# Performance work log

Measured on AMD Instinct MI355X. Metric: run time of the kernel, lower is better.

Reference implementation:

```python
import jax, jax.numpy as jnp
import numpy as np

NEG = -9e15
ALPHA = 0.2  # leaky relu slope

def setup_inputs() -> dict:
    key = jax.random.key(0)
    k1, k2, k3, k4 = jax.random.split(key, 4)
    N, Fin, Fout = 8192, 512, 256
    h = jax.random.normal(k1, (N, Fin), dtype=jnp.float32)
    adj = jax.random.randint(k2, (N, N), 0, 2, dtype=jnp.int32)
    # xavier_uniform with gain=1.414
    gain = 1.414
    limW = gain * np.sqrt(6.0 / (Fin + Fout))
    W = jax.random.uniform(k3, (Fin, Fout), dtype=jnp.float32, minval=-limW, maxval=limW)
    lima = gain * np.sqrt(6.0 / (2 * Fout + 1))
    a = jax.random.uniform(k4, (2 * Fout, 1), dtype=jnp.float32, minval=-lima, maxval=lima)
    return {"h": h, "adj": adj, "W": W, "a": a}

def reference(h, adj, W, a):
    Fout = W.shape[1]
    Wh = h @ W                                   # [N, Fout]
    # decompose a = [a1; a2]: e_ij = leaky(a1.Wh_i + a2.Wh_j)
    f1 = Wh @ a[:Fout]                           # [N, 1]
    f2 = Wh @ a[Fout:]                           # [N, 1]
    e = jax.nn.leaky_relu(f1 + f2.T, negative_slope=ALPHA)  # [N, N]
    e = jnp.where(adj > 0, e, jnp.float32(NEG))
    attention = jax.nn.softmax(e, axis=1)
    # dropout is identity at inference (training=False)
    h_prime = attention @ Wh                     # [N, Fout]
    return jax.nn.elu(h_prime)
```

## Files before the change

### kernel.cpp

```cpp
#include <hip/hip_runtime.h>
#include <cstdint>
#include <cstddef>

#define ALPHA 0.2f

typedef __attribute__((ext_vector_type(8)))  short short8;
typedef __attribute__((ext_vector_type(16))) float f32x16;

static __device__ __forceinline__ unsigned short f2bf(float x) {
  union { float f; unsigned u; } c; c.f = x;
  unsigned u = c.u;
  unsigned r = (u + 0x7FFFu + ((u >> 16) & 1u)) >> 16;
  return (unsigned short)r;
}
static __device__ __forceinline__ float bf2f(unsigned short b) {
  union { unsigned u; float f; } c; c.u = ((unsigned)b) << 16;
  return c.f;
}

__global__ __launch_bounds__(256, 2) void gemm1(const float* __restrict__ h,
                                                const float* __restrict__ W,
                                                float* __restrict__ Wh) {
  __shared__ float As[32][132];
  __shared__ float Bs[32][64];
  const int t = threadIdx.x;
  const int bid = blockIdx.x;
  const int nb = bid & 3, mb = bid >> 2;
  const int m0 = mb * 128, n0 = nb * 64;
  const int ty = t >> 4, tx = t & 15;
  float acc[8][4];
#pragma unroll
  for (int i = 0; i < 8; i++)
#pragma unroll
    for (int j = 0; j < 4; j++) acc[i][j] = 0.f;

  for (int k0 = 0; k0 < 512; k0 += 32) {
#pragma unroll
    for (int c = 0; c < 4; c++) {
      int m = c * 32 + (t >> 3);
      int kq = (t & 7) * 4;
      float4 v = *(const float4*)&h[(size_t)(m0 + m) * 512 + k0 + kq];
      As[kq + 0][m] = v.x; As[kq + 1][m] = v.y;
      As[kq + 2][m] = v.z; As[kq + 3][m] = v.w;
    }
#pragma unroll
    for (int c = 0; c < 2; c++) {
      int k = c * 16 + (t >> 4);
      int n = (t & 15) * 4;
      *(float4*)&Bs[k][n] = *(const float4*)&W[(size_t)(k0 + k) * 256 + n0 + n];
    }
    __syncthreads();
#pragma unroll
    for (int k = 0; k < 32; k++) {
      float4 a0 = *(float4*)&As[k][ty * 8];
      float4 a1 = *(float4*)&As[k][ty * 8 + 4];
      float4 b  = *(float4*)&Bs[k][tx * 4];
      float av[8] = {a0.x, a0.y, a0.z, a0.w, a1.x, a1.y, a1.z, a1.w};
      float bv[4] = {b.x, b.y, b.z, b.w};
#pragma unroll
      for (int i = 0; i < 8; i++)
#pragma unroll
        for (int j = 0; j < 4; j++) acc[i][j] = fmaf(av[i], bv[j], acc[i][j]);
    }
    __syncthreads();
  }
#pragma unroll
  for (int i = 0; i < 8; i++) {
    float4 v = {acc[i][0], acc[i][1], acc[i][2], acc[i][3]};
    *(float4*)&Wh[(size_t)(m0 + ty * 8 + i) * 256 + n0 + tx * 4] = v;
  }
}

__global__ __launch_bounds__(256) void rowstats(const float* __restrict__ Wh,
                                                const float* __restrict__ a,
                                                float* __restrict__ f1,
                                                float* __restrict__ f2,
                                                unsigned* __restrict__ uvpack) {
  const int t = threadIdx.x;
  const int w = t >> 6, lane = t & 63;
  const int i = blockIdx.x * 4 + w;
  float4 wv = *(const float4*)&Wh[(size_t)i * 256 + lane * 4];
  float4 a1 = *(const float4*)&a[lane * 4];
  float4 a2 = *(const float4*)&a[256 + lane * 4];
  float s1 = wv.x * a1.x + wv.y * a1.y + wv.z * a1.z + wv.w * a1.w;
  float s2 = wv.x * a2.x + wv.y * a2.y + wv.z * a2.z + wv.w * a2.w;
#pragma unroll
  for (int off = 32; off; off >>= 1) { s1 += __shfl_xor(s1, off); s2 += __shfl_xor(s2, off); }
  if (lane == 0) {
    f1[i] = s1; f2[i] = s2;
    float u = __expf(s2), v = __expf(ALPHA * s2);
    uvpack[i] = (unsigned)f2bf(u) | ((unsigned)f2bf(v) << 16);
  }
}

__global__ __launch_bounds__(256) void wtrans(const float* __restrict__ Wh,
                                              unsigned short* __restrict__ WhT) {
  __shared__ unsigned short T[64][80];
  const int t = threadIdx.x;
  const int bi = blockIdx.x & 127;
  const int bc = blockIdx.x >> 7;
  const int i0 = bi * 64, c0 = bc * 64;
  {
    const int il = t >> 2, cq = (t & 3) * 16;
#pragma unroll
    for (int k = 0; k < 4; ++k) {
      float4 v = *(const float4*)&Wh[(size_t)(i0 + il) * 256 + c0 + cq + k * 4];
      T[cq + k * 4 + 0][il] = f2bf(v.x);
      T[cq + k * 4 + 1][il] = f2bf(v.y);
      T[cq + k * 4 + 2][il] = f2bf(v.z);
      T[cq + k * 4 + 3][il] = f2bf(v.w);
    }
  }
  __syncthreads();
  {
    const int cl = t >> 2, iq = (t & 3) * 16;
    *(uint4*)&WhT[(size_t)(c0 + cl) * 8192 + i0 + iq]     = *(const uint4*)&T[cl][iq];
    *(uint4*)&WhT[(size_t)(c0 + cl) * 8192 + i0 + iq + 8] = *(const uint4*)&T[cl][iq + 8];
  }
}

__global__ __launch_bounds__(256) void f2max_k(const float* __restrict__ f2,
                                               float* __restrict__ f2maxp) {
  __shared__ float red[256];
  const int t = threadIdx.x;
  float m = -1e30f;
  for (int c = 0; c < 32; c++) m = fmaxf(m, f2[c * 256 + t]);
  red[t] = m;
  __syncthreads();
  for (int s = 128; s; s >>= 1) {
    if (t < s) red[t] = fmaxf(red[t], red[t + s]);
    __syncthreads();
  }
  if (t == 0) f2maxp[0] = red[0];
}

#define ATTN_PHASE(S_CUR, A0, A1, U0, U1, BF_CUR, BF_NXT)                        \
  {                                                                              \
    const int ad_[8] = {A0.x, A0.y, A0.z, A0.w, A1.x, A1.y, A1.z, A1.w};         \
    const unsigned uu_[8] = {U0.x, U0.y, U0.z, U0.w, U1.x, U1.y, U1.z, U1.w};    \
    float w_[8];                                                                 \
    _Pragma("unroll")                                                            \
    for (int jj = 0; jj < 8; jj++) {                                             \
      float u = bf2f((unsigned short)(uu_[jj] & 0xFFFFu));                       \
      float v = bf2f((unsigned short)(uu_[jj] >> 16));                           \
      float wv = (u > Ui) ? Ai * u : Bi * v;                                     \
      w_[jj] = (ad_[jj] > 0) ? wv : 0.f;                                         \
    }                                                                            \
    lpriv += ((w_[0] + w_[1]) + (w_[2] + w_[3])) + ((w_[4] + w_[5]) + (w_[6] + w_[7])); \
    union { uint4 q; short8 s; } af_;                                            \
    asm("v_cvt_pk_bf16_f32 %0, %1, %2" : "=v"(af_.q.x) : "v"(w_[0]), "v"(w_[1]));\
    asm("v_cvt_pk_bf16_f32 %0, %1, %2" : "=v"(af_.q.y) : "v"(w_[2]), "v"(w_[3]));\
    asm("v_cvt_pk_bf16_f32 %0, %1, %2" : "=v"(af_.q.z) : "v"(w_[4]), "v"(w_[5]));\
    asm("v_cvt_pk_bf16_f32 %0, %1, %2" : "=v"(af_.q.w) : "v"(w_[6]), "v"(w_[7]));\
    const int sRe_ = (S_CUR) + 2;                                                \
    if (sRe_ < 128) {                                                            \
      A0 = *(const int4*)(adjp + sRe_ * 16);                                     \
      A1 = *(const int4*)(adjp + sRe_ * 16 + 4);                                 \
      U0 = *(const uint4*)(uvp + sRe_ * 16);                                     \
      U1 = *(const uint4*)(uvp + sRe_ * 16 + 4);                                 \
    }                                                                            \
    const int sN_ = (S_CUR) + 1;                                                 \
    if (sN_ < 128) {                                                             \
      _Pragma("unroll")                                                          \
      for (int ct = 0; ct < 8; ct++)                                             \
        BF_NXT[ct] = *(const short8*)(wtp + (size_t)ct * (32 * 8192) + sN_ * 16);\
    }                                                                            \
    _Pragma("unroll")                                                            \
    for (int ct = 0; ct < 8; ct++)                                               \
      acc[ct] = __builtin_amdgcn_mfma_f32_32x32x16_bf16(af_.s, BF_CUR[ct], acc[ct], 0, 0, 0); \
  }

__global__ __launch_bounds__(256, 1) void attn_main(const int* __restrict__ adj,
                                                    const float* __restrict__ f1,
                                                    const unsigned* __restrict__ uvpack,
                                                    const unsigned short* __restrict__ WhT,
                                                    const float* __restrict__ f2maxp,
                                                    float* __restrict__ out) {
  __shared__ float red[4][32][260];
  __shared__ float lsum[4][32];
  const int t = threadIdx.x;
  const int wave = t >> 6, lane = t & 63;
  const int am = lane & 31, asel = lane >> 5;
  const int r0 = blockIdx.x * 32;
  const int row = r0 + am;
  const int jq = wave * 2048;
  const int joff = jq + asel * 8;

  const float F2max = f2maxp[0];
  const float f1v = f1[row];
  const float x = f1v + F2max;
  const float M = x > 0.f ? x : ALPHA * x;
  const float Ai = __expf(f1v - M);
  const float Bi = __expf(ALPHA * f1v - M);
  const float Ui = __expf(-f1v);

  f32x16 acc[8] = {};
  const int* adjp = adj + (size_t)row * 8192 + joff;
  const unsigned* uvp = uvpack + joff;
  const unsigned short* wtp = WhT + (size_t)am * 8192 + joff;

  int4 aA0 = *(const int4*)(adjp);
  int4 aA1 = *(const int4*)(adjp + 4);
  uint4 uA0 = *(const uint4*)(uvp);
  uint4 uA1 = *(const uint4*)(uvp + 4);
  int4 aB0 = *(const int4*)(adjp + 16);
  int4 aB1 = *(const int4*)(adjp + 20);
  uint4 uB0 = *(const uint4*)(uvp + 16);
  uint4 uB1 = *(const uint4*)(uvp + 20);
  short8 bfA[8], bfB[8];
#pragma unroll
  for (int ct = 0; ct < 8; ct++)
    bfA[ct] = *(const short8*)(wtp + (size_t)ct * (32 * 8192));
  float lpriv = 0.f;

#pragma unroll 1
  for (int it = 0; it < 64; ++it) {
    ATTN_PHASE(2 * it,     aA0, aA1, uA0, uA1, bfA, bfB);
    ATTN_PHASE(2 * it + 1, aB0, aB1, uB0, uB1, bfB, bfA);
  }

#pragma unroll
  for (int ct = 0; ct < 8; ct++) {
#pragma unroll
    for (int reg = 0; reg < 16; reg++) {
      const int rowl = (reg & 3) + 8 * (reg >> 2) + 4 * asel;
      red[wave][rowl][ct * 32 + am] = acc[ct][reg];
    }
  }
  lpriv += __shfl_xor(lpriv, 32);
  if (asel == 0) lsum[wave][am] = lpriv;
  __syncthreads();

  const int rr = t >> 3, cb = (t & 7) * 32;
  const float l = lsum[0][rr] + lsum[1][rr] + lsum[2][rr] + lsum[3][rr];
  const float inv = 1.0f / fmaxf(l, 1e-30f);
#pragma unroll
  for (int cc = 0; cc < 32; cc += 4) {
    float4 v;
    v.x = red[0][rr][cb + cc + 0] + red[1][rr][cb + cc + 0] + red[2][rr][cb + cc + 0] + red[3][rr][cb + cc + 0];
    v.y = red[0][rr][cb + cc + 1] + red[1][rr][cb + cc + 1] + red[2][rr][cb + cc + 1] + red[3][rr][cb + cc + 1];
    v.z = red[0][rr][cb + cc + 2] + red[1][rr][cb + cc + 2] + red[2][rr][cb + cc + 2] + red[3][rr][cb + cc + 2];
    v.w = red[0][rr][cb + cc + 3] + red[1][rr][cb + cc + 3] + red[2][rr][cb + cc + 3] + red[3][rr][cb + cc + 3];
    v.x *= inv; v.y *= inv; v.z *= inv; v.w *= inv;
    float4 o;
    o.x = v.x > 0.f ? v.x : __expf(v.x) - 1.f;
    o.y = v.y > 0.f ? v.y : __expf(v.y) - 1.f;
    o.z = v.z > 0.f ? v.z : __expf(v.z) - 1.f;
    o.w = v.w > 0.f ? v.w : __expf(v.w) - 1.f;
    *(float4*)&out[(size_t)(r0 + rr) * 256 + cb + cc] = o;
  }
}

extern "C" void kernel_launch(void* const* d_in, const int* in_sizes, int n_in,
                              void* d_out, int out_size, void* d_ws, size_t ws_size,
                              hipStream_t stream) {
  const float* h  = (const float*)d_in[0];
  const int* adj  = (const int*)d_in[1];
  const float* W  = (const float*)d_in[2];
  const float* a  = (const float*)d_in[3];
  float* out = (float*)d_out;
  char* ws = (char*)d_ws;

  float* Wh            = (float*)ws;
  unsigned short* WhT  = (unsigned short*)(ws + (size_t)(16u << 20));
  float* f1            = (float*)(ws + (size_t)(20u << 20));
  float* f2            = (float*)(ws + (size_t)(20u << 20) + (32u << 10));
  unsigned* uvpack     = (unsigned*)(ws + (size_t)(20u << 20) + (64u << 10));
  float* f2maxp        = (float*)(ws + (size_t)(20u << 20) + (96u << 10));

  gemm1<<<256, 256, 0, stream>>>(h, W, Wh);
  rowstats<<<2048, 256, 0, stream>>>(Wh, a, f1, f2, uvpack);
  wtrans<<<512, 256, 0, stream>>>(Wh, WhT);
  f2max_k<<<1, 256, 0, stream>>>(f2, f2maxp);
  attn_main<<<256, 256, 0, stream>>>(adj, f1, uvpack, WhT, f2maxp, out);
}
```

Before: 570.4 us.

## Pre-pack adjacency into bitmask, restructure attention loop, and widen gemm1 blocks

A new maskpack kernel reads the int32 adjacency once with coalesced loads and ballots it into a 64-bit-per-64-column bitmask. attn_main then streams this compact mask instead of 32-bit adj values, and applies it with bit-extract and AND instead of compares. The attention loop is regrouped into four-step groups with prefetched mask and uvpack data, and the WhT prefetch is clamped rather than guarded. gemm1 moves to 512 threads per block with a 4x4 per-thread tile. The full adj read (256 MB) still happens once in maskpack, so the gain depends on attn_main having been limited by scattered adj loads rather than total bandwidth.

```diff
diff --git a/kernel.cpp b/kernel.cpp
--- a/kernel.cpp
+++ b/kernel.cpp
@@ -13,14 +13,10 @@
   unsigned r = (u + 0x7FFFu + ((u >> 16) & 1u)) >> 16;
   return (unsigned short)r;
 }
-static __device__ __forceinline__ float bf2f(unsigned short b) {
-  union { unsigned u; float f; } c; c.u = ((unsigned)b) << 16;
-  return c.f;
-}
-
-__global__ __launch_bounds__(256, 2) void gemm1(const float* __restrict__ h,
-                                                const float* __restrict__ W,
-                                                float* __restrict__ Wh) {
+
+__global__ __launch_bounds__(512) void gemm1(const float* __restrict__ h,
+                                             const float* __restrict__ W,
+                                             float* __restrict__ Wh) {
   __shared__ float As[32][132];
   __shared__ float Bs[32][64];
   const int t = threadIdx.x;
@@ -28,46 +24,44 @@
   const int nb = bid & 3, mb = bid >> 2;
   const int m0 = mb * 128, n0 = nb * 64;
   const int ty = t >> 4, tx = t & 15;
-  float acc[8][4];
-#pragma unroll
-  for (int i = 0; i < 8; i++)
+  float acc[4][4];
+#pragma unroll
+  for (int i = 0; i < 4; i++)
 #pragma unroll
     for (int j = 0; j < 4; j++) acc[i][j] = 0.f;
 
   for (int k0 = 0; k0 < 512; k0 += 32) {
 #pragma unroll
-    for (int c = 0; c < 4; c++) {
-      int m = c * 32 + (t >> 3);
+    for (int c = 0; c < 2; c++) {
+      int m = c * 64 + (t >> 3);
       int kq = (t & 7) * 4;
       float4 v = *(const float4*)&h[(size_t)(m0 + m) * 512 + k0 + kq];
       As[kq + 0][m] = v.x; As[kq + 1][m] = v.y;
       As[kq + 2][m] = v.z; As[kq + 3][m] = v.w;
     }
-#pragma unroll
-    for (int c = 0; c < 2; c++) {
-      int k = c * 16 + (t >> 4);
+    {
+      int k = t >> 4;
       int n = (t & 15) * 4;
       *(float4*)&Bs[k][n] = *(const float4*)&W[(size_t)(k0 + k) * 256 + n0 + n];
     }
     __syncthreads();
 #pragma unroll
     for (int k = 0; k < 32; k++) {
-      float4 a0 = *(float4*)&As[k][ty * 8];
-      float4 a1 = *(float4*)&As[k][ty * 8 + 4];
-      float4 b  = *(float4*)&Bs[k][tx * 4];
-      float av[8] = {a0.x, a0.y, a0.z, a0.w, a1.x, a1.y, a1.z, a1.w};
+      float4 a = *(float4*)&As[k][ty * 4];
+      float4 b = *(float4*)&Bs[k][tx * 4];
+      float av[4] = {a.x, a.y, a.z, a.w};
       float bv[4] = {b.x, b.y, b.z, b.w};
 #pragma unroll
-      for (int i = 0; i < 8; i++)
+      for (int i = 0; i < 4; i++)
 #pragma unroll
         for (int j = 0; j < 4; j++) acc[i][j] = fmaf(av[i], bv[j], acc[i][j]);
     }
     __syncthreads();
   }
 #pragma unroll
-  for (int i = 0; i < 8; i++) {
+  for (int i = 0; i < 4; i++) {
     float4 v = {acc[i][0], acc[i][1], acc[i][2], acc[i][3]};
-    *(float4*)&Wh[(size_t)(m0 + ty * 8 + i) * 256 + n0 + tx * 4] = v;
+    *(float4*)&Wh[(size_t)(m0 + ty * 4 + i) * 256 + n0 + tx * 4] = v;
   }
 }
 
@@ -134,17 +128,46 @@
   if (t == 0) f2maxp[0] = red[0];
 }
 
-#define ATTN_PHASE(S_CUR, A0, A1, U0, U1, BF_CUR, BF_NXT)                        \
+__global__ __launch_bounds__(256) void maskpack(const int* __restrict__ adj,
+                                                unsigned long long* __restrict__ mask) {
+  __shared__ unsigned long long mbuf[4][128];
+  const int t = threadIdx.x, wave = t >> 6, lane = t & 63;
+  const int row = blockIdx.x * 4 + wave;
+  const int* ap = adj + (size_t)row * 8192 + lane;
+#pragma unroll 1
+  for (int it0 = 0; it0 < 128; it0 += 4) {
+    int a0 = ap[(it0 + 0) * 64];
+    int a1 = ap[(it0 + 1) * 64];
+    int a2 = ap[(it0 + 2) * 64];
+    int a3 = ap[(it0 + 3) * 64];
+    unsigned long long b0 = __ballot(a0 > 0);
+    unsigned long long b1 = __ballot(a1 > 0);
+    unsigned long long b2 = __ballot(a2 > 0);
+    unsigned long long b3 = __ballot(a3 > 0);
+    if (lane == 0) {
+      mbuf[wave][it0 + 0] = b0; mbuf[wave][it0 + 1] = b1;
+      mbuf[wave][it0 + 2] = b2; mbuf[wave][it0 + 3] = b3;
+    }
+  }
+  __syncthreads();
+  uint4* dst = (uint4*)(mask + (size_t)blockIdx.x * 4 * 128);
+  dst[t] = ((const uint4*)mbuf)[t];
+}
+
+#define ATTN_SUB(KSUB, MWORD, UCA, UCB, BFC, BFN, SCUR)                          \
   {                                                                              \
-    const int ad_[8] = {A0.x, A0.y, A0.z, A0.w, A1.x, A1.y, A1.z, A1.w};         \
-    const unsigned uu_[8] = {U0.x, U0.y, U0.z, U0.w, U1.x, U1.y, U1.z, U1.w};    \
+    const unsigned mbyte_ = ((MWORD) >> (((KSUB) & 1) * 16 + aselsh)) & 0xFFu;   \
+    const unsigned uu_[8] = {UCA.x, UCA.y, UCA.z, UCA.w, UCB.x, UCB.y, UCB.z, UCB.w}; \
     float w_[8];                                                                 \
     _Pragma("unroll")                                                            \
     for (int jj = 0; jj < 8; jj++) {                                             \
-      float u = bf2f((unsigned short)(uu_[jj] & 0xFFFFu));                       \
-      float v = bf2f((unsigned short)(uu_[jj] >> 16));                           \
-      float wv = (u > Ui) ? Ai * u : Bi * v;                                     \
-      w_[jj] = (ad_[jj] > 0) ? wv : 0.f;                                         \
+      union { unsigned u; float f; } cu_, cv_;                                   \
+      cu_.u = uu_[jj] << 16;                                                     \
+      cv_.u = uu_[jj] & 0xFFFF0000u;                                             \
+      float wv_ = (cu_.f > Ui) ? Ai * cu_.f : Bi * cv_.f;                        \
+      int ext_ = ((int)(mbyte_ << (31 - jj))) >> 31;    \
+      union { float f; int i; } wu_; wu_.f = wv_; wu_.i &= ext_;                 \
+      w_[jj] = wu_.f;                                                            \
     }                                                                            \
     lpriv += ((w_[0] + w_[1]) + (w_[2] + w_[3])) + ((w_[4] + w_[5]) + (w_[6] + w_[7])); \
     union { uint4 q; short8 s; } af_;                                            \
@@ -152,25 +175,34 @@
     asm("v_cvt_pk_bf16_f32 %0, %1, %2" : "=v"(af_.q.y) : "v"(w_[2]), "v"(w_[3]));\
     asm("v_cvt_pk_bf16_f32 %0, %1, %2" : "=v"(af_.q.z) : "v"(w_[4]), "v"(w_[5]));\
     asm("v_cvt_pk_bf16_f32 %0, %1, %2" : "=v"(af_.q.w) : "v"(w_[6]), "v"(w_[7]));\
-    const int sRe_ = (S_CUR) + 2;                                                \
-    if (sRe_ < 128) {                                                            \
-      A0 = *(const int4*)(adjp + sRe_ * 16);                                     \
-      A1 = *(const int4*)(adjp + sRe_ * 16 + 4);                                 \
-      U0 = *(const uint4*)(uvp + sRe_ * 16);                                     \
-      U1 = *(const uint4*)(uvp + sRe_ * 16 + 4);                                 \
-    }                                                                            \
-    const int sN_ = (S_CUR) + 1;                                                 \
-    if (sN_ < 128) {                                                             \
-      _Pragma("unroll")                                                          \
-      for (int ct = 0; ct < 8; ct++)                                             \
-        BF_NXT[ct] = *(const short8*)(wtp + (size_t)ct * (32 * 8192) + sN_ * 16);\
-    }                                                                            \
+    const int sn_ = (SCUR) + 1 < 128 ? (SCUR) + 1 : 127;                         \
     _Pragma("unroll")                                                            \
     for (int ct = 0; ct < 8; ct++)                                               \
-      acc[ct] = __builtin_amdgcn_mfma_f32_32x32x16_bf16(af_.s, BF_CUR[ct], acc[ct], 0, 0, 0); \
-  }
-
-__global__ __launch_bounds__(256, 1) void attn_main(const int* __restrict__ adj,
+      BFN[ct] = *(const short8*)(wtp + (size_t)ct * (32 * 8192) + (size_t)sn_ * 16); \
+    _Pragma("unroll")                                                            \
+    for (int ct = 0; ct < 8; ct++)                                               \
+      acc[ct] = __builtin_amdgcn_mfma_f32_32x32x16_bf16(af_.s, BFC[ct], acc[ct], 0, 0, 0); \
+  }
+
+#define ATTN_GROUP(G, UC, UN, MC, MN)                                            \
+  {                                                                              \
+    const int gn_ = (G) < 31 ? (G) + 1 : 31;                                     \
+    MN = mp[gn_];                                                                \
+    UN[0] = *(const uint4*)(uvp + gn_ * 64 + 0);                                 \
+    UN[1] = *(const uint4*)(uvp + gn_ * 64 + 4);                                 \
+    ATTN_SUB(0, MC.x, UC[0], UC[1], bfA, bfB, 4 * (G) + 0);                      \
+    UN[2] = *(const uint4*)(uvp + gn_ * 64 + 16);                                \
+    UN[3] = *(const uint4*)(uvp + gn_ * 64 + 20);                                \
+    ATTN_SUB(1, MC.x, UC[2], UC[3], bfB, bfA, 4 * (G) + 1);                      \
+    UN[4] = *(const uint4*)(uvp + gn_ * 64 + 32);                                \
+    UN[5] = *(const uint4*)(uvp + gn_ * 64 + 36);                                \
+    ATTN_SUB(2, MC.y, UC[4], UC[5], bfA, bfB, 4 * (G) + 2);                      \
+    UN[6] = *(const uint4*)(uvp + gn_ * 64 + 48);                                \
+    UN[7] = *(const uint4*)(uvp + gn_ * 64 + 52);                                \
+    ATTN_SUB(3, MC.y, UC[6], UC[7], bfB, bfA, 4 * (G) + 3);                      \
+  }
+
+__global__ __launch_bounds__(256, 1) void attn_main(const unsigned long long* __restrict__ maskw,
                                                     const float* __restrict__ f1,
                                                     const unsigned* __restrict__ uvpack,
                                                     const unsigned short* __restrict__ WhT,
@@ -181,10 +213,10 @@
   const int t = threadIdx.x;
   const int wave = t >> 6, lane = t & 63;
   const int am = lane & 31, asel = lane >> 5;
+  const int aselsh = asel * 8;
   const int r0 = blockIdx.x * 32;
   const int row = r0 + am;
   const int jq = wave * 2048;
-  const int joff = jq + asel * 8;
 
   const float F2max = f2maxp[0];
   const float f1v = f1[row];
@@ -195,18 +227,17 @@
   const float Ui = __expf(-f1v);
 
   f32x16 acc[8] = {};
-  const int* adjp = adj + (size_t)row * 8192 + joff;
-  const unsigned* uvp = uvpack + joff;
-  const unsigned short* wtp = WhT + (size_t)am * 8192 + joff;
-
-  int4 aA0 = *(const int4*)(adjp);
-  int4 aA1 = *(const int4*)(adjp + 4);
-  uint4 uA0 = *(const uint4*)(uvp);
-  uint4 uA1 = *(const uint4*)(uvp + 4);
-  int4 aB0 = *(const int4*)(adjp + 16);
-  int4 aB1 = *(const int4*)(adjp + 20);
-  uint4 uB0 = *(const uint4*)(uvp + 16);
-  uint4 uB1 = *(const uint4*)(uvp + 20);
+  const uint2* mp = (const uint2*)maskw + (size_t)row * 128 + wave * 32;
+  const unsigned* uvp = uvpack + jq + aselsh;
+  const unsigned short* wtp = WhT + (size_t)am * 8192 + jq + aselsh;
+
+  uint2 mg = mp[0], mgN;
+  uint4 ug[8], ugN[8];
+#pragma unroll
+  for (int k = 0; k < 4; k++) {
+    ug[2 * k]     = *(const uint4*)(uvp + k * 16);
+    ug[2 * k + 1] = *(const uint4*)(uvp + k * 16 + 4);
+  }
   short8 bfA[8], bfB[8];
 #pragma unroll
   for (int ct = 0; ct < 8; ct++)
@@ -214,9 +245,9 @@
   float lpriv = 0.f;
 
 #pragma unroll 1
-  for (int it = 0; it < 64; ++it) {
-    ATTN_PHASE(2 * it,     aA0, aA1, uA0, uA1, bfA, bfB);
-    ATTN_PHASE(2 * it + 1, aB0, aB1, uB0, uB1, bfB, bfA);
+  for (int gg = 0; gg < 16; ++gg) {
+    ATTN_GROUP(2 * gg,     ug,  ugN, mg,  mgN);
+    ATTN_GROUP(2 * gg + 1, ugN, ug,  mgN, mg);
   }
 
 #pragma unroll
@@ -262,15 +293,17 @@
   char* ws = (char*)d_ws;
 
   float* Wh            = (float*)ws;
+  unsigned long long* mask = (unsigned long long*)(ws + (size_t)(8u << 20));
   unsigned short* WhT  = (unsigned short*)(ws + (size_t)(16u << 20));
   float* f1            = (float*)(ws + (size_t)(20u << 20));
   float* f2            = (float*)(ws + (size_t)(20u << 20) + (32u << 10));
   unsigned* uvpack     = (unsigned*)(ws + (size_t)(20u << 20) + (64u << 10));
   float* f2maxp        = (float*)(ws + (size_t)(20u << 20) + (96u << 10));
 
-  gemm1<<<256, 256, 0, stream>>>(h, W, Wh);
+  maskpack<<<2048, 256, 0, stream>>>(adj, mask);
+  gemm1<<<256, 512, 0, stream>>>(h, W, Wh);
   rowstats<<<2048, 256, 0, stream>>>(Wh, a, f1, f2, uvpack);
   wtrans<<<512, 256, 0, stream>>>(Wh, WhT);
   f2max_k<<<1, 256, 0, stream>>>(f2, f2maxp);
-  attn_main<<<256, 256, 0, stream>>>(adj, f1, uvpack, WhT, f2maxp, out);
-}
+  attn_main<<<256, 256, 0, stream>>>(mask, f1, uvpack, WhT, f2maxp, out);
+}
```

Result: faster. 548.9 us (-3.8%).
